# Kernel tuning notes

Hardware: AMD Instinct MI355X
Metric: run time of the kernel (lower is better)

## Reference

```python
import jax, jax.numpy as jnp
import numpy as np

VOCAB = 50257
SMALL = 512
LARGE = 1024
B, S = 4, 2048


def setup_inputs() -> dict:
    key = jax.random.key(0)
    k1, k2, k3, k4 = jax.random.split(key, 4)
    input_ids = jax.random.randint(k1, (B, S), 0, VOCAB)
    weight = jax.random.normal(k2, (VOCAB, SMALL), dtype=jnp.float32) * 0.02
    # coeffs_weight stored as (large-small, small); init like normalized uniform
    cw = jax.random.uniform(k3, (LARGE - SMALL, SMALL), dtype=jnp.float32)
    coeffs_weight = cw / jnp.sum(cw, axis=-1, keepdims=True)
    residual_weight = jax.random.uniform(k4, (VOCAB, LARGE), dtype=jnp.float32,
                                         minval=-0.01, maxval=0.01)
    return {"input_ids": input_ids, "weight": weight,
            "coeffs_weight": coeffs_weight, "residual_weight": residual_weight}


def reference(input_ids, weight, coeffs_weight, residual_weight):
    # get_params(): expand width then add residual over the FULL vocab
    # expanded part: weight @ coeffs_weight.T -> (vocab, large-small)
    expanded = jnp.matmul(weight, coeffs_weight.T)
    full = jnp.concatenate([weight, expanded], axis=1) + residual_weight  # (vocab, large)
    # F.embedding gather
    return jnp.take(full, input_ids, axis=0)  # (B, S, large)
```

## Files before the change

kernel.cpp:

```cpp
#include <hip/hip_runtime.h>
#include <hip/hip_bf16.h>

typedef __attribute__((ext_vector_type(8))) short bf16x8;
typedef __attribute__((ext_vector_type(4))) float f32x4;

constexpr int SMALL = 512;
constexpr int LARGE = 1024;
constexpr int NTOK  = 4 * 2048;
constexpr int TPB   = 32;
constexpr int LDA   = SMALL + 8;

static __device__ __forceinline__ unsigned short f2bf(float f) {
    __hip_bfloat16 h = __float2bfloat16(f);
    return *reinterpret_cast<unsigned short*>(&h);
}

__global__ __launch_bounds__(256) void k_cvt_coeffs(const float* __restrict__ coeffs,
                                                    unsigned short* __restrict__ b_bf16) {
    int i = blockIdx.x * 256 + threadIdx.x;
    int e = i << 2;
    const float4 cvec = *reinterpret_cast<const float4*>(coeffs + e);
    ushort4 b;
    b.x = f2bf(cvec.x); b.y = f2bf(cvec.y); b.z = f2bf(cvec.z); b.w = f2bf(cvec.w);
    *reinterpret_cast<ushort4*>(b_bf16 + e) = b;
}

__global__ __launch_bounds__(512) void k_fused(const int* __restrict__ ids,
                                               const float* __restrict__ weight,
                                               const float* __restrict__ residual,
                                               const unsigned short* __restrict__ B,
                                               float* __restrict__ out) {
    __shared__ unsigned short As[TPB * LDA];
    __shared__ int s_ids[TPB];

    const int tid  = threadIdx.x;
    const int tok0 = blockIdx.x * TPB;

    if (tid < TPB) s_ids[tid] = ids[tok0 + tid];
    __syncthreads();

    {
        const int t  = tid & 31;
        const int c0 = (tid >> 5) * 32;
        const int id = s_ids[t];
        const float* wrow = weight   + (size_t)id * SMALL + c0;
        const float* rrow = residual + (size_t)id * LARGE + c0;
        float*       orow = out + (size_t)(tok0 + t) * LARGE + c0;
        unsigned short* arow = As + t * LDA + c0;
#pragma unroll
        for (int j = 0; j < 8; ++j) {
            const float4 w = *reinterpret_cast<const float4*>(wrow + 4 * j);
            const float4 r = *reinterpret_cast<const float4*>(rrow + 4 * j);
            float4 o;
            o.x = w.x + r.x; o.y = w.y + r.y; o.z = w.z + r.z; o.w = w.w + r.w;
            *reinterpret_cast<float4*>(orow + 4 * j) = o;
            ushort4 a;
            a.x = f2bf(w.x); a.y = f2bf(w.y); a.z = f2bf(w.z); a.w = f2bf(w.w);
            *reinterpret_cast<ushort4*>(arow + 4 * j) = a;
        }
    }
    __syncthreads();

    const int wv   = tid >> 6;
    const int lane = tid & 63;
    const int r0   = (wv & 1) * 16;
    const int c0b  = (wv >> 1) * 128;
    const int lr   = lane & 15;
    const int lk   = (lane >> 4) * 8;

    f32x4 acc[8] = {};
    const unsigned short* a_addr = As + (r0 + lr) * LDA + lk;
    const unsigned short* pb     = B + (size_t)(c0b + lr) * SMALL + lk;

    for (int k0 = 0; k0 < 512; k0 += 32) {
        const bf16x8 a = *reinterpret_cast<const bf16x8*>(a_addr + k0);
#pragma unroll
        for (int n = 0; n < 8; ++n) {
            const bf16x8 b = *reinterpret_cast<const bf16x8*>(pb + (size_t)n * 16 * SMALL + k0);
            acc[n] = __builtin_amdgcn_mfma_f32_16x16x32_bf16(a, b, acc[n], 0, 0, 0);
        }
    }

    const int rloc = r0 + (lane >> 4) * 4;
#pragma unroll
    for (int r = 0; r < 4; ++r) {
        const int trow = rloc + r;
        const int id2  = s_ids[trow];
        const float* res = residual + (size_t)id2 * LARGE + SMALL + c0b + lr;
        float*       op  = out + (size_t)(tok0 + trow) * LARGE + SMALL + c0b + lr;
#pragma unroll
        for (int n = 0; n < 8; ++n)
            op[n * 16] = acc[n][r] + res[n * 16];
    }
}

extern "C" void kernel_launch(void* const* d_in, const int* in_sizes, int n_in,
                              void* d_out, int out_size, void* d_ws, size_t ws_size,
                              hipStream_t stream) {
    const int*   ids      = (const int*)d_in[0];
    const float* weight   = (const float*)d_in[1];
    const float* coeffs   = (const float*)d_in[2];
    const float* residual = (const float*)d_in[3];
    float*       out      = (float*)d_out;

    unsigned short* b_bf16 = (unsigned short*)d_ws;

    k_cvt_coeffs<<<(512 * 128) / 256, 256, 0, stream>>>(coeffs, b_bf16);
    k_fused<<<NTOK / TPB, 512, 0, stream>>>(ids, weight, residual, b_bf16, out);
}
```

Baseline: 339.2 us.

## Coalesce row loads, stage residual tail in LDS, halve tokens per block

```diff
diff --git a/kernel.cpp b/kernel.cpp
--- a/kernel.cpp
+++ b/kernel.cpp
@@ -7,8 +7,9 @@
 constexpr int SMALL = 512;
 constexpr int LARGE = 1024;
 constexpr int NTOK  = 4 * 2048;
-constexpr int TPB   = 32;
+constexpr int TPB   = 16;
 constexpr int LDA   = SMALL + 8;
+constexpr int LDR   = SMALL + 4;
 
 static __device__ __forceinline__ unsigned short f2bf(float f) {
     __hip_bfloat16 h = __float2bfloat16(f);
@@ -25,12 +26,13 @@
     *reinterpret_cast<ushort4*>(b_bf16 + e) = b;
 }
 
-__global__ __launch_bounds__(512) void k_fused(const int* __restrict__ ids,
+__global__ __launch_bounds__(256) void k_fused(const int* __restrict__ ids,
                                                const float* __restrict__ weight,
                                                const float* __restrict__ residual,
                                                const unsigned short* __restrict__ B,
                                                float* __restrict__ out) {
     __shared__ unsigned short As[TPB * LDA];
+    __shared__ float          Rs[TPB * LDR];
     __shared__ int s_ids[TPB];
 
     const int tid  = threadIdx.x;
@@ -40,36 +42,43 @@
     __syncthreads();
 
     {
-        const int t  = tid & 31;
-        const int c0 = (tid >> 5) * 32;
-        const int id = s_ids[t];
-        const float* wrow = weight   + (size_t)id * SMALL + c0;
-        const float* rrow = residual + (size_t)id * LARGE + c0;
-        float*       orow = out + (size_t)(tok0 + t) * LARGE + c0;
-        unsigned short* arow = As + t * LDA + c0;
+        const int t   = tid >> 4;
+        const int sub = tid & 15;
+        const int id  = s_ids[t];
+        const float* wrow = weight   + (size_t)id * SMALL;
+        const float* rrow = residual + (size_t)id * LARGE;
+        float*       orow = out + (size_t)(tok0 + t) * LARGE;
+        unsigned short* arow = As + t * LDA;
+        float*          rsrw = Rs + t * LDR;
 #pragma unroll
         for (int j = 0; j < 8; ++j) {
-            const float4 w = *reinterpret_cast<const float4*>(wrow + 4 * j);
-            const float4 r = *reinterpret_cast<const float4*>(rrow + 4 * j);
+            const int c = j * 64 + sub * 4;
+            const float4 w = *reinterpret_cast<const float4*>(wrow + c);
+            const float4 r = *reinterpret_cast<const float4*>(rrow + c);
             float4 o;
             o.x = w.x + r.x; o.y = w.y + r.y; o.z = w.z + r.z; o.w = w.w + r.w;
-            *reinterpret_cast<float4*>(orow + 4 * j) = o;
+            *reinterpret_cast<float4*>(orow + c) = o;
             ushort4 a;
             a.x = f2bf(w.x); a.y = f2bf(w.y); a.z = f2bf(w.z); a.w = f2bf(w.w);
-            *reinterpret_cast<ushort4*>(arow + 4 * j) = a;
+            *reinterpret_cast<ushort4*>(arow + c) = a;
+        }
+#pragma unroll
+        for (int j = 0; j < 8; ++j) {
+            const int c = j * 64 + sub * 4;
+            const float4 r = *reinterpret_cast<const float4*>(rrow + SMALL + c);
+            *reinterpret_cast<float4*>(rsrw + c) = r;
         }
     }
     __syncthreads();
 
     const int wv   = tid >> 6;
     const int lane = tid & 63;
-    const int r0   = (wv & 1) * 16;
-    const int c0b  = (wv >> 1) * 128;
+    const int c0b  = wv * 128;
     const int lr   = lane & 15;
     const int lk   = (lane >> 4) * 8;
 
     f32x4 acc[8] = {};
-    const unsigned short* a_addr = As + (r0 + lr) * LDA + lk;
+    const unsigned short* a_addr = As + lr * LDA + lk;
     const unsigned short* pb     = B + (size_t)(c0b + lr) * SMALL + lk;
 
     for (int k0 = 0; k0 < 512; k0 += 32) {
@@ -81,16 +90,15 @@
         }
     }
 
-    const int rloc = r0 + (lane >> 4) * 4;
+    const int rloc = (lane >> 4) * 4;
 #pragma unroll
     for (int r = 0; r < 4; ++r) {
         const int trow = rloc + r;
-        const int id2  = s_ids[trow];
-        const float* res = residual + (size_t)id2 * LARGE + SMALL + c0b + lr;
         float*       op  = out + (size_t)(tok0 + trow) * LARGE + SMALL + c0b + lr;
+        const float* rs  = Rs + trow * LDR + c0b + lr;
 #pragma unroll
         for (int n = 0; n < 8; ++n)
-            op[n * 16] = acc[n][r] + res[n * 16];
+            op[n * 16] = acc[n][r] + rs[n * 16];
     }
 }
 
@@ -106,5 +114,5 @@
     unsigned short* b_bf16 = (unsigned short*)d_ws;
 
     k_cvt_coeffs<<<(512 * 128) / 256, 256, 0, stream>>>(coeffs, b_bf16);
-    k_fused<<<NTOK / TPB, 512, 0, stream>>>(ids, weight, residual, b_bf16, out);
+    k_fused<<<NTOK / TPB, 256, 0, stream>>>(ids, weight, residual, b_bf16, out);
 }
```

Result: faster. 328.5 us (-3.1%).
